# Optimization experiments

Hardware: AMD Instinct MI355X
Metric: run time of the kernel (lower is better)

## Reference

```python
import jax, jax.numpy as jnp
import numpy as np

B, S, D, H = 4, 2048, 1024, 16
HD = D // H


def setup_inputs() -> dict:
    key = jax.random.key(0)
    ks = jax.random.split(key, 10)
    x = jax.random.normal(ks[0], (B, S, D), dtype=jnp.float32)
    mask = jnp.zeros((B, 1, 1, S), dtype=jnp.float32)  # 1 = masked, 0 = keep
    sc = 1.0 / np.sqrt(D)
    wq = jax.random.normal(ks[1], (D, D), dtype=jnp.float32) * sc
    wk = jax.random.normal(ks[2], (D, D), dtype=jnp.float32) * sc
    wv = jax.random.normal(ks[3], (D, D), dtype=jnp.float32) * sc
    wo = jax.random.normal(ks[4], (D, D), dtype=jnp.float32) * sc
    bq = jnp.zeros((D,), jnp.float32)
    bk = jnp.zeros((D,), jnp.float32)
    bv = jnp.zeros((D,), jnp.float32)
    bo = jnp.zeros((D,), jnp.float32)
    return {"x": x, "mask": mask, "wq": wq, "bq": bq, "wk": wk, "bk": bk,
            "wv": wv, "bv": bv, "wo": wo, "bo": bo}


def _split_heads(t):
    # (B, S, D) -> (B, H, S, HD)
    return t.reshape(B, -1, H, HD).transpose(0, 2, 1, 3)


def reference(x, mask, wq, bq, wk, bk, wv, bv, wo, bo):
    q = _split_heads(x @ wq + bq)
    k = _split_heads(x @ wk + bk)
    v = _split_heads(x @ wv + bv)
    # scaled dot-product attention (TF tutorial convention: mask*-1e9 added)
    scores = jnp.einsum("bhqd,bhkd->bhqk", q, k) / jnp.sqrt(jnp.float32(HD))
    scores = scores + mask * -1e9
    attn_weights = jax.nn.softmax(scores, axis=-1)  # (B, H, Sq, Sk)
    attn = jnp.einsum("bhqk,bhkd->bhqd", attn_weights, v)
    attn = attn.transpose(0, 2, 1, 3).reshape(B, -1, D)
    out = attn @ wo + bo
    return out, attn_weights
```

## Files before the change

kernel.cpp:

```cpp
#include <hip/hip_runtime.h>
#include <hip/hip_bf16.h>

#define S_LEN  2048
#define DMODEL 1024
#define NHEAD  16
#define HDIM   64
#define BSZ    4

#define C_SCORE  0.18033688f
#define C_MASK  -1.4426950e9f

typedef __bf16 bf16_t;
typedef __bf16 bf16x8 __attribute__((ext_vector_type(8)));
typedef __bf16 bf16x4 __attribute__((ext_vector_type(4)));
typedef float  f32x4  __attribute__((ext_vector_type(4)));

typedef __attribute__((address_space(1))) void as1_void;
typedef __attribute__((address_space(3))) void as3_void;

__device__ __forceinline__ f32x4 mfma16(bf16x8 a, bf16x8 b, f32x4 c) {
    return __builtin_amdgcn_mfma_f32_16x16x32_bf16(a, b, c, 0, 0, 0);
}

__global__ __launch_bounds__(256) void cvt_all(const float* __restrict__ x,
                                               bf16_t* __restrict__ xb,
                                               const float* __restrict__ w0,
                                               const float* __restrict__ w1,
                                               const float* __restrict__ w2,
                                               const float* __restrict__ w3,
                                               bf16_t* __restrict__ wT) {
    __shared__ bf16_t t[64][65];
    const int bid = blockIdx.x;
    if (bid < 4096) {
        const int i0 = bid * 256 + threadIdx.x;
        #pragma unroll
        for (int rep = 0; rep < 2; ++rep) {
            const int i = i0 + rep * 1048576;
            float4 v = ((const float4*)x)[i];
            bf16x4 tv = { (bf16_t)v.x, (bf16_t)v.y, (bf16_t)v.z, (bf16_t)v.w };
            ((bf16x4*)xb)[i] = tv;
        }
        return;
    }
    const int wb = bid - 4096;
    const int wsel = wb >> 8;
    const float* w = wsel == 0 ? w0 : (wsel == 1 ? w1 : (wsel == 2 ? w2 : w3));
    bf16_t* wTo = wT + (size_t)wsel * DMODEL * DMODEL;
    const int rb = wb & 255;
    const int bx = (rb & 15) * 64, by = (rb >> 4) * 64;
    const int tx = threadIdx.x & 63, ty = threadIdx.x >> 6;
    #pragma unroll
    for (int rr = 0; rr < 64; rr += 4)
        t[tx][rr + ty] = (bf16_t)w[(size_t)(bx + rr + ty) * DMODEL + by + tx];
    __syncthreads();
    #pragma unroll
    for (int rr = 0; rr < 64; rr += 4)
        wTo[(size_t)(by + rr + ty) * DMODEL + bx + tx] = t[rr + ty][tx];
}

template <int MODE>
__global__ __launch_bounds__(256) void gemm_bt(const bf16_t* __restrict__ A,
                                               const bf16_t* __restrict__ Bt,
                                               const float* __restrict__ b0,
                                               const float* __restrict__ b1,
                                               const float* __restrict__ b2,
                                               bf16_t* __restrict__ o0,
                                               bf16_t* __restrict__ o1,
                                               bf16_t* __restrict__ o2,
                                               float* __restrict__ of) {
    constexpr int GK = 1024;
    __shared__ __attribute__((aligned(16))) bf16_t smem_ab[8704];
    bf16_t* As = smem_ab;
    bf16_t* Bs = smem_ab + 4096;

    const int tid  = threadIdx.x;
    const int wave = tid >> 6, lane = tid & 63;
    const int col16 = lane & 15, g = lane >> 4;
    const int wr = wave >> 1, wc = wave & 1;
    const int bn0 = blockIdx.x * 128, bm0 = blockIdx.y * 128;

    const int r4 = tid >> 2;
    const int c8 = (tid & 3) * 8;

    f32x4 acc[4][4] = {};

    for (int k0 = 0; k0 < GK; k0 += 32) {
        __syncthreads();
        #pragma unroll
        for (int i = 0; i < 2; ++i) {
            __builtin_amdgcn_global_load_lds(
                (const as1_void*)(A + (size_t)(bm0 + i * 64 + r4) * GK + k0 + c8),
                (as3_void*)(As + (i * 64 + wave * 16) * 32), 16, 0, 0);
            __builtin_amdgcn_global_load_lds(
                (const as1_void*)(Bt + (size_t)(bn0 + i * 64 + r4) * GK + k0 + c8),
                (as3_void*)(Bs + (i * 64 + wave * 16) * 32), 16, 0, 0);
        }
        __syncthreads();

        bf16x8 af[4], bfr[4];
        #pragma unroll
        for (int i = 0; i < 4; ++i) {
            af[i]  = *(const bf16x8*)(As + (wr * 64 + i * 16 + col16) * 32 + g * 8);
            bfr[i] = *(const bf16x8*)(Bs + (wc * 64 + i * 16 + col16) * 32 + g * 8);
        }
        #pragma unroll
        for (int mi = 0; mi < 4; ++mi)
            #pragma unroll
            for (int ni = 0; ni < 4; ++ni)
                acc[mi][ni] = mfma16(af[mi], bfr[ni], acc[mi][ni]);
    }

    if (MODE == 0 && (bn0 >> 10) == 2) {
        const int n1base = bn0 - 2048;
        const int brow = bm0 >> 11;
        const int s0 = bm0 & 2047;
        __syncthreads();
        #pragma unroll
        for (int p = 0; p < 2; ++p) {
            if (p) __syncthreads();
            if (wc == p) {
                #pragma unroll
                for (int ni = 0; ni < 4; ++ni) {
                    const float bv = b2[n1base + p * 64 + ni * 16 + col16];
                    #pragma unroll
                    for (int mi = 0; mi < 4; ++mi) {
                        bf16x4 pv;
                        #pragma unroll
                        for (int r = 0; r < 4; ++r) pv[r] = (bf16_t)(acc[mi][ni][r] + bv);
                        *(bf16x4*)&smem_ab[(ni * 16 + col16) * 136 + wr * 64 + mi * 16 + g * 4] = pv;
                    }
                }
            }
            __syncthreads();
            const int h2 = (n1base + p * 64) >> 6;
            bf16_t* vout = o2 + (((size_t)brow * NHEAD + h2) * HDIM) * S_LEN + s0;
            #pragma unroll
            for (int j = 0; j < 4; ++j) {
                const int unit = j * 256 + tid;
                const int row = unit >> 4;
                const int cu = (unit & 15) * 8;
                bf16x8 v = *(const bf16x8*)&smem_ab[row * 136 + cu];
                *(bf16x8*)(vout + (size_t)row * S_LEN + cu) = v;
            }
        }
        return;
    }

    #pragma unroll
    for (int ni = 0; ni < 4; ++ni) {
        const int gn = bn0 + wc * 64 + ni * 16 + col16;
        if (MODE == 0) {
            const int proj = bn0 >> 10;
            const float* bias = proj == 0 ? b0 : b1;
            bf16_t* outp      = proj == 0 ? o0 : o1;
            const int n1 = gn & 1023, h = n1 >> 6, hd = n1 & 63;
            const float bv = bias[n1];
            #pragma unroll
            for (int mi = 0; mi < 4; ++mi)
                #pragma unroll
                for (int r = 0; r < 4; ++r) {
                    const int gm = bm0 + wr * 64 + mi * 16 + g * 4 + r;
                    const int b = gm >> 11, s = gm & 2047;
                    outp[(((size_t)b * NHEAD + h) * S_LEN + s) * HDIM + hd] =
                        (bf16_t)(acc[mi][ni][r] + bv);
                }
        } else {
            const float bv = b0[gn];
            #pragma unroll
            for (int mi = 0; mi < 4; ++mi)
                #pragma unroll
                for (int r = 0; r < 4; ++r) {
                    const int gm = bm0 + wr * 64 + mi * 16 + g * 4 + r;
                    of[(size_t)gm * DMODEL + gn] = acc[mi][ni][r] + bv;
                }
        }
    }
}

__global__ __launch_bounds__(256, 2) void attn_fused(const bf16_t* __restrict__ Q,
                                                     const bf16_t* __restrict__ K,
                                                     const bf16_t* __restrict__ Vt,
                                                     const float* __restrict__ mask,
                                                     float* __restrict__ attnW,
                                                     bf16_t* __restrict__ ctx) {
    __shared__ __attribute__((aligned(16))) char smem[73728];
    bf16_t (*KsA)[128][64] = (bf16_t(*)[128][64])smem;
    bf16_t (*Ks)[64][64]   = (bf16_t(*)[64][64])smem;
    bf16_t (*Vs)[64][64]   = (bf16_t(*)[64][64])(smem + 16384);
    float  (*Pl)[32][64]   = (float(*)[32][64])(smem + 32768);
    float*  Ml             = (float*)(smem + 65536);

    const int tid = threadIdx.x, wave = tid >> 6, lane = tid & 63;
    const int col16 = lane & 15, g = lane >> 4;
    const int r7 = col16 & 7;

    const int lin = blockIdx.x;
    const int logical = (lin & 7) * 64 + (lin >> 3);
    const int bh = logical >> 3, pp = logical & 7;
    const int b = bh >> 4, h = bh & 15;
    const int qA = pp * 256 + wave * 32;
    const int qB = pp * 256 + 128 + wave * 32;

    const bf16_t* Qb = Q + (size_t)bh * S_LEN * HDIM;
    const bf16_t* Kb = K + (size_t)bh * S_LEN * HDIM;
    const bf16_t* Vb = Vt + (size_t)bh * HDIM * S_LEN;
    const float* mp = mask + (size_t)b * S_LEN;

    #pragma unroll
    for (int i = 0; i < 2; ++i) {
        const int idx = i * 256 + tid;
        f32x4 v = ((const f32x4*)mp)[idx];
        #pragma unroll
        for (int r = 0; r < 4; ++r) v[r] *= C_MASK;
        *(f32x4*)(&Ml[idx * 4]) = v;
    }

    const int srow  = lane >> 3;
    const int sunit = (lane & 7) ^ srow;

    auto stageA = [&](int buf, int it) {
        const int kk0 = it << 7;
        #pragma unroll
        for (int i2 = 0; i2 < 4; ++i2) {
            const int i = wave * 4 + i2;
            __builtin_amdgcn_global_load_lds(
                (const as1_void*)(Kb + (size_t)(kk0 + i * 8 + srow) * HDIM + sunit * 8),
                (as3_void*)(&KsA[buf][i * 8][0]), 16, 0, 0);
        }
    };
    auto stageK = [&](int buf, int it) {
        const int kk0 = it << 6;
        #pragma unroll
        for (int i2 = 0; i2 < 2; ++i2) {
            const int i = wave * 2 + i2;
            __builtin_amdgcn_global_load_lds(
                (const as1_void*)(Kb + (size_t)(kk0 + i * 8 + srow) * HDIM + sunit * 8),
                (as3_void*)(&Ks[buf][i * 8][0]), 16, 0, 0);
        }
    };
    auto stageV = [&](int buf, int it) {
        const int kk0 = it << 6;
        #pragma unroll
        for (int i2 = 0; i2 < 2; ++i2) {
            const int i = wave * 2 + i2;
            __builtin_amdgcn_global_load_lds(
                (const as1_void*)(Vb + (size_t)(i * 8 + srow) * S_LEN + kk0 + sunit * 8),
                (as3_void*)(&Vs[buf][i * 8][0]), 16, 0, 0);
        }
    };
    auto kfrag = [&](int buf, int nj, int kh) {
        return *(const bf16x8*)(&Ks[buf][nj * 16 + col16][(((kh * 4 + g) ^ r7) * 8)]);
    };
    auto vfrag = [&](int buf, int nd, int kh) {
        return *(const bf16x8*)(&Vs[buf][nd * 16 + col16][(((kh * 4 + g) ^ r7) * 8)]);
    };

    bf16x8 qa0[2][2], qa1[2][2];
    #pragma unroll
    for (int hh = 0; hh < 2; ++hh)
        #pragma unroll
        for (int kh = 0; kh < 2; ++kh) {
            qa0[hh][kh] = *(const bf16x8*)(Qb + (size_t)(qA + hh * 16 + col16) * HDIM +
                                           kh * 32 + g * 8);
            qa1[hh][kh] = *(const bf16x8*)(Qb + (size_t)(qB + hh * 16 + col16) * HDIM +
                                           kh * 32 + g * 8);
        }

    f32x4 lacc0[2] = {}, lacc1[2] = {};
    stageA(0, 0);
    __syncthreads();

    for (int it = 0; it < 16; ++it) {
        const int kk0 = it << 7, cur = it & 1;
        if (it < 15) stageA(cur ^ 1, it + 1);
        #pragma unroll
        for (int nj = 0; nj < 8; ++nj) {
            const f32x4 mvr = *(const f32x4*)(&Ml[kk0 + nj * 16 + g * 4]);
            const bf16x8 kf0 = *(const bf16x8*)(&KsA[cur][nj * 16 + col16][((g ^ r7) * 8)]);
            const bf16x8 kf1 = *(const bf16x8*)(&KsA[cur][nj * 16 + col16][(((4 + g) ^ r7) * 8)]);
            f32x4 t0 = {0.f, 0.f, 0.f, 0.f}, t1 = {0.f, 0.f, 0.f, 0.f};
            f32x4 u0 = {0.f, 0.f, 0.f, 0.f}, u1 = {0.f, 0.f, 0.f, 0.f};
            t0 = mfma16(kf0, qa0[0][0], t0);
            t0 = mfma16(kf1, qa0[0][1], t0);
            t1 = mfma16(kf0, qa0[1][0], t1);
            t1 = mfma16(kf1, qa0[1][1], t1);
            u0 = mfma16(kf0, qa1[0][0], u0);
            u0 = mfma16(kf1, qa1[0][1], u0);
            u1 = mfma16(kf0, qa1[1][0], u1);
            u1 = mfma16(kf1, qa1[1][1], u1);
            #pragma unroll
            for (int r = 0; r < 4; ++r) {
                lacc0[0][r] += exp2f(fmaf(t0[r], C_SCORE, mvr[r]));
                lacc0[1][r] += exp2f(fmaf(t1[r], C_SCORE, mvr[r]));
                lacc1[0][r] += exp2f(fmaf(u0[r], C_SCORE, mvr[r]));
                lacc1[1][r] += exp2f(fmaf(u1[r], C_SCORE, mvr[r]));
            }
        }
        asm volatile("s_waitcnt vmcnt(0)" ::: "memory");
        __builtin_amdgcn_sched_barrier(0);
        __builtin_amdgcn_s_barrier();
    }

    float crow0[2], crow1[2];
    #pragma unroll
    for (int hh = 0; hh < 2; ++hh) {
        float lr0 = (lacc0[hh][0] + lacc0[hh][1]) + (lacc0[hh][2] + lacc0[hh][3]);
        lr0 += __shfl_xor(lr0, 16);
        lr0 += __shfl_xor(lr0, 32);
        crow0[hh] = -__log2f(lr0);
        float lr1 = (lacc1[hh][0] + lacc1[hh][1]) + (lacc1[hh][2] + lacc1[hh][3]);
        lr1 += __shfl_xor(lr1, 16);
        lr1 += __shfl_xor(lr1, 32);
        crow1[hh] = -__log2f(lr1);
    }

    f32x4 o0[2][4] = {}, o1[2][4] = {};
    float* awA = attnW + ((size_t)bh * S_LEN + qA) * S_LEN;
    float* awB = attnW + ((size_t)bh * S_LEN + qB) * S_LEN;

    stageK(0, 0);
    stageV(0, 0);
    asm volatile("s_waitcnt vmcnt(0)" ::: "memory");
    __builtin_amdgcn_sched_barrier(0);
    __builtin_amdgcn_s_barrier();

    for (int it = 0; it < 32; ++it) {
        const int kk0 = it << 6, cur = it & 1;
        if (it < 31) { stageK(cur ^ 1, it + 1); stageV(cur ^ 1, it + 1); }
        __builtin_amdgcn_sched_barrier(0);
        f32x4 mvr[4];
        #pragma unroll
        for (int nj = 0; nj < 4; ++nj)
            mvr[nj] = *(const f32x4*)(&Ml[kk0 + nj * 16 + g * 4]);

        #pragma unroll
        for (int nj = 0; nj < 4; ++nj) {
            const bf16x8 kf0 = kfrag(cur, nj, 0);
            const bf16x8 kf1 = kfrag(cur, nj, 1);
            f32x4 s0 = {0.f, 0.f, 0.f, 0.f}, s1 = {0.f, 0.f, 0.f, 0.f};
            s0 = mfma16(kf0, qa0[0][0], s0);
            s0 = mfma16(kf1, qa0[0][1], s0);
            s1 = mfma16(kf0, qa0[1][0], s1);
            s1 = mfma16(kf1, qa0[1][1], s1);
            f32x4 pn0, pn1;
            #pragma unroll
            for (int r = 0; r < 4; ++r) {
                const float mm = mvr[nj][r];
                pn0[r] = exp2f(fmaf(s0[r], C_SCORE, mm + crow0[0]));
                pn1[r] = exp2f(fmaf(s1[r], C_SCORE, mm + crow0[1]));
            }
            const int pw = ((nj * 4 + g) ^ r7) * 4;
            *(f32x4*)(&Pl[wave][col16][pw])      = pn0;
            *(f32x4*)(&Pl[wave][16 + col16][pw]) = pn1;
        }
        #pragma unroll
        for (int j = 0; j < 8; ++j) {
            const int row = j * 4 + (lane >> 4);
            const int u = lane & 15;
            const f32x4 v = *(const f32x4*)(&Pl[wave][row][((u ^ (row & 7)) * 4)]);
            __builtin_nontemporal_store(v, (f32x4*)(awA + (size_t)row * S_LEN + kk0 + u * 4));
        }
        #pragma unroll
        for (int hh = 0; hh < 2; ++hh)
            #pragma unroll
            for (int kh = 0; kh < 2; ++kh) {
                const int u0i = kh * 8 + g * 2;
                const f32x4 a0 = *(const f32x4*)(&Pl[wave][hh * 16 + col16][((u0i ^ r7) * 4)]);
                const f32x4 a1 = *(const f32x4*)(&Pl[wave][hh * 16 + col16][(((u0i + 1) ^ r7) * 4)]);
                bf16x8 pa;
                #pragma unroll
                for (int j = 0; j < 4; ++j) {
                    pa[j]     = (bf16_t)a0[j];
                    pa[4 + j] = (bf16_t)a1[j];
                }
                #pragma unroll
                for (int nd = 0; nd < 4; ++nd)
                    o0[hh][nd] = mfma16(vfrag(cur, nd, kh), pa, o0[hh][nd]);
            }

        #pragma unroll
        for (int nj = 0; nj < 4; ++nj) {
            const bf16x8 kf0 = kfrag(cur, nj, 0);
            const bf16x8 kf1 = kfrag(cur, nj, 1);
            f32x4 s0 = {0.f, 0.f, 0.f, 0.f}, s1 = {0.f, 0.f, 0.f, 0.f};
            s0 = mfma16(kf0, qa1[0][0], s0);
            s0 = mfma16(kf1, qa1[0][1], s0);
            s1 = mfma16(kf0, qa1[1][0], s1);
            s1 = mfma16(kf1, qa1[1][1], s1);
            f32x4 pn0, pn1;
            #pragma unroll
            for (int r = 0; r < 4; ++r) {
                const float mm = mvr[nj][r];
                pn0[r] = exp2f(fmaf(s0[r], C_SCORE, mm + crow1[0]));
                pn1[r] = exp2f(fmaf(s1[r], C_SCORE, mm + crow1[1]));
            }
            const int pw = ((nj * 4 + g) ^ r7) * 4;
            *(f32x4*)(&Pl[wave][col16][pw])      = pn0;
            *(f32x4*)(&Pl[wave][16 + col16][pw]) = pn1;
        }
        #pragma unroll
        for (int j = 0; j < 8; ++j) {
            const int row = j * 4 + (lane >> 4);
            const int u = lane & 15;
            const f32x4 v = *(const f32x4*)(&Pl[wave][row][((u ^ (row & 7)) * 4)]);
            __builtin_nontemporal_store(v, (f32x4*)(awB + (size_t)row * S_LEN + kk0 + u * 4));
        }
        #pragma unroll
        for (int hh = 0; hh < 2; ++hh)
            #pragma unroll
            for (int kh = 0; kh < 2; ++kh) {
                const int u0i = kh * 8 + g * 2;
                const f32x4 a0 = *(const f32x4*)(&Pl[wave][hh * 16 + col16][((u0i ^ r7) * 4)]);
                const f32x4 a1 = *(const f32x4*)(&Pl[wave][hh * 16 + col16][(((u0i + 1) ^ r7) * 4)]);
                bf16x8 pa;
                #pragma unroll
                for (int j = 0; j < 4; ++j) {
                    pa[j]     = (bf16_t)a0[j];
                    pa[4 + j] = (bf16_t)a1[j];
                }
                #pragma unroll
                for (int nd = 0; nd < 4; ++nd)
                    o1[hh][nd] = mfma16(vfrag(cur, nd, kh), pa, o1[hh][nd]);
            }

        asm volatile("s_waitcnt vmcnt(16)" ::: "memory");
        __builtin_amdgcn_sched_barrier(0);
        __builtin_amdgcn_s_barrier();
    }

    #pragma unroll
    for (int hh = 0; hh < 2; ++hh) {
        bf16_t* cpA = ctx + ((size_t)b * S_LEN + qA + hh * 16 + col16) * DMODEL + h * HDIM;
        bf16_t* cpB = ctx + ((size_t)b * S_LEN + qB + hh * 16 + col16) * DMODEL + h * HDIM;
        #pragma unroll
        for (int nd = 0; nd < 4; ++nd) {
            bf16x4 cv0, cv1;
            #pragma unroll
            for (int r = 0; r < 4; ++r) {
                cv0[r] = (bf16_t)o0[hh][nd][r];
                cv1[r] = (bf16_t)o1[hh][nd][r];
            }
            *(bf16x4*)(cpA + nd * 16 + g * 4) = cv0;
            *(bf16x4*)(cpB + nd * 16 + g * 4) = cv1;
        }
    }
}

extern "C" void kernel_launch(void* const* d_in, const int* in_sizes, int n_in,
                              void* d_out, int out_size, void* d_ws, size_t ws_size,
                              hipStream_t stream) {
    const float* x    = (const float*)d_in[0];
    const float* mask = (const float*)d_in[1];
    const float* wq   = (const float*)d_in[2];
    const float* bq   = (const float*)d_in[3];
    const float* wk   = (const float*)d_in[4];
    const float* bk   = (const float*)d_in[5];
    const float* wv   = (const float*)d_in[6];
    const float* bv   = (const float*)d_in[7];
    const float* wo   = (const float*)d_in[8];
    const float* bo   = (const float*)d_in[9];

    const size_t nX = (size_t)BSZ * S_LEN * DMODEL;
    const size_t nW = (size_t)DMODEL * DMODEL;

    char* ws = (char*)d_ws;
    size_t off = 0;
    bf16_t* xb     = (bf16_t*)(ws + off); off += nX * 2;
    bf16_t* wqkvT  = (bf16_t*)(ws + off); off += 3 * nW * 2;
    bf16_t* woT    = (bf16_t*)(ws + off); off += nW * 2;
    bf16_t* qbh    = (bf16_t*)(ws + off); off += nX * 2;
    bf16_t* kbh    = (bf16_t*)(ws + off); off += nX * 2;
    bf16_t* vtb    = (bf16_t*)(ws + off); off += nX * 2;
    bf16_t* ctx    = (bf16_t*)(ws + off); off += nX * 2;
    if (ws_size < off) return;

    float* outp  = (float*)d_out;
    float* attnW = outp + nX;

    cvt_all<<<5120, 256, 0, stream>>>(x, xb, wq, wk, wv, wo, wqkvT);

    gemm_bt<0><<<dim3(24, 64), 256, 0, stream>>>(xb, wqkvT, bq, bk, bv,
                                                 qbh, kbh, vtb, nullptr);

    attn_fused<<<512, 256, 0, stream>>>(qbh, kbh, vtb, mask, attnW, ctx);

    gemm_bt<2><<<dim3(8, 64), 256, 0, stream>>>(ctx, woT, bo, nullptr, nullptr,
                                                nullptr, nullptr, nullptr, outp);
}
```

Measured before the change: 379.2 us.

## Split attention work across 8 waves with 16 query rows each

Doubles the attention block to 512 threads so each wave handles 16 query rows per half instead of 32. Global-to-LDS staging of K, V and the mask is spread across the eight waves, and the vmcnt wait is adjusted to match. The aim is lower per-wave register pressure and more waves to hide latency and overlap MFMA with exp work. The cost is that each K/V fragment read from LDS now feeds fewer MFMAs, raising LDS traffic. The tighter launch bounds also risk register spills.

New measurement: 369.0 us. 1.03x faster.

```diff
diff --git a/kernel.cpp b/kernel.cpp
--- a/kernel.cpp
+++ b/kernel.cpp
@@ -177,7 +177,7 @@
     }
 }
 
-__global__ __launch_bounds__(256, 2) void attn_fused(const bf16_t* __restrict__ Q,
+__global__ __launch_bounds__(512, 4) void attn_fused(const bf16_t* __restrict__ Q,
                                                      const bf16_t* __restrict__ K,
                                                      const bf16_t* __restrict__ Vt,
                                                      const float* __restrict__ mask,
@@ -187,7 +187,7 @@
     bf16_t (*KsA)[128][64] = (bf16_t(*)[128][64])smem;
     bf16_t (*Ks)[64][64]   = (bf16_t(*)[64][64])smem;
     bf16_t (*Vs)[64][64]   = (bf16_t(*)[64][64])(smem + 16384);
-    float  (*Pl)[32][64]   = (float(*)[32][64])(smem + 32768);
+    float  (*Pl)[16][64]   = (float(*)[16][64])(smem + 32768);
     float*  Ml             = (float*)(smem + 65536);
 
     const int tid = threadIdx.x, wave = tid >> 6, lane = tid & 63;
@@ -198,21 +198,19 @@
     const int logical = (lin & 7) * 64 + (lin >> 3);
     const int bh = logical >> 3, pp = logical & 7;
     const int b = bh >> 4, h = bh & 15;
-    const int qA = pp * 256 + wave * 32;
-    const int qB = pp * 256 + 128 + wave * 32;
+    const int qA = pp * 256 + wave * 16;
+    const int qB = pp * 256 + 128 + wave * 16;
 
     const bf16_t* Qb = Q + (size_t)bh * S_LEN * HDIM;
     const bf16_t* Kb = K + (size_t)bh * S_LEN * HDIM;
     const bf16_t* Vb = Vt + (size_t)bh * HDIM * S_LEN;
     const float* mp = mask + (size_t)b * S_LEN;
 
-    #pragma unroll
-    for (int i = 0; i < 2; ++i) {
-        const int idx = i * 256 + tid;
-        f32x4 v = ((const f32x4*)mp)[idx];
+    {
+        f32x4 v = ((const f32x4*)mp)[tid];
         #pragma unroll
         for (int r = 0; r < 4; ++r) v[r] *= C_MASK;
-        *(f32x4*)(&Ml[idx * 4]) = v;
+        *(f32x4*)(&Ml[tid * 4]) = v;
     }
 
     const int srow  = lane >> 3;
@@ -220,33 +218,25 @@
 
     auto stageA = [&](int buf, int it) {
         const int kk0 = it << 7;
-        #pragma unroll
-        for (int i2 = 0; i2 < 4; ++i2) {
-            const int i = wave * 4 + i2;
-            __builtin_amdgcn_global_load_lds(
-                (const as1_void*)(Kb + (size_t)(kk0 + i * 8 + srow) * HDIM + sunit * 8),
-                (as3_void*)(&KsA[buf][i * 8][0]), 16, 0, 0);
-        }
-    };
-    auto stageK = [&](int buf, int it) {
-        const int kk0 = it << 6;
         #pragma unroll
         for (int i2 = 0; i2 < 2; ++i2) {
             const int i = wave * 2 + i2;
             __builtin_amdgcn_global_load_lds(
                 (const as1_void*)(Kb + (size_t)(kk0 + i * 8 + srow) * HDIM + sunit * 8),
-                (as3_void*)(&Ks[buf][i * 8][0]), 16, 0, 0);
-        }
+                (as3_void*)(&KsA[buf][i * 8][0]), 16, 0, 0);
+        }
+    };
+    auto stageK = [&](int buf, int it) {
+        const int kk0 = it << 6;
+        __builtin_amdgcn_global_load_lds(
+            (const as1_void*)(Kb + (size_t)(kk0 + wave * 8 + srow) * HDIM + sunit * 8),
+            (as3_void*)(&Ks[buf][wave * 8][0]), 16, 0, 0);
     };
     auto stageV = [&](int buf, int it) {
         const int kk0 = it << 6;
-        #pragma unroll
-        for (int i2 = 0; i2 < 2; ++i2) {
-            const int i = wave * 2 + i2;
-            __builtin_amdgcn_global_load_lds(
-                (const as1_void*)(Vb + (size_t)(i * 8 + srow) * S_LEN + kk0 + sunit * 8),
-                (as3_void*)(&Vs[buf][i * 8][0]), 16, 0, 0);
-        }
+        __builtin_amdgcn_global_load_lds(
+            (const as1_void*)(Vb + (size_t)(wave * 8 + srow) * S_LEN + kk0 + sunit * 8),
+            (as3_void*)(&Vs[buf][wave * 8][0]), 16, 0, 0);
     };
     auto kfrag = [&](int buf, int nj, int kh) {
         return *(const bf16x8*)(&Ks[buf][nj * 16 + col16][(((kh * 4 + g) ^ r7) * 8)]);
@@ -255,18 +245,14 @@
         return *(const bf16x8*)(&Vs[buf][nd * 16 + col16][(((kh * 4 + g) ^ r7) * 8)]);
     };
 
-    bf16x8 qa0[2][2], qa1[2][2];
+    bf16x8 qa0[2], qa1[2];
     #pragma unroll
-    for (int hh = 0; hh < 2; ++hh)
-        #pragma unroll
-        for (int kh = 0; kh < 2; ++kh) {
-            qa0[hh][kh] = *(const bf16x8*)(Qb + (size_t)(qA + hh * 16 + col16) * HDIM +
-                                           kh * 32 + g * 8);
-            qa1[hh][kh] = *(const bf16x8*)(Qb + (size_t)(qB + hh * 16 + col16) * HDIM +
-                                           kh * 32 + g * 8);
-        }
-
-    f32x4 lacc0[2] = {}, lacc1[2] = {};
+    for (int kh = 0; kh < 2; ++kh) {
+        qa0[kh] = *(const bf16x8*)(Qb + (size_t)(qA + col16) * HDIM + kh * 32 + g * 8);
+        qa1[kh] = *(const bf16x8*)(Qb + (size_t)(qB + col16) * HDIM + kh * 32 + g * 8);
+    }
+
+    f32x4 lacc0 = {}, lacc1 = {};
     stageA(0, 0);
     __syncthreads();
 
@@ -278,22 +264,15 @@
             const f32x4 mvr = *(const f32x4*)(&Ml[kk0 + nj * 16 + g * 4]);
             const bf16x8 kf0 = *(const bf16x8*)(&KsA[cur][nj * 16 + col16][((g ^ r7) * 8)]);
             const bf16x8 kf1 = *(const bf16x8*)(&KsA[cur][nj * 16 + col16][(((4 + g) ^ r7) * 8)]);
-            f32x4 t0 = {0.f, 0.f, 0.f, 0.f}, t1 = {0.f, 0.f, 0.f, 0.f};
-            f32x4 u0 = {0.f, 0.f, 0.f, 0.f}, u1 = {0.f, 0.f, 0.f, 0.f};
-            t0 = mfma16(kf0, qa0[0][0], t0);
-            t0 = mfma16(kf1, qa0[0][1], t0);
-            t1 = mfma16(kf0, qa0[1][0], t1);
-            t1 = mfma16(kf1, qa0[1][1], t1);
-            u0 = mfma16(kf0, qa1[0][0], u0);
-            u0 = mfma16(kf1, qa1[0][1], u0);
-            u1 = mfma16(kf0, qa1[1][0], u1);
-            u1 = mfma16(kf1, qa1[1][1], u1);
+            f32x4 t0 = {0.f, 0.f, 0.f, 0.f}, u0 = {0.f, 0.f, 0.f, 0.f};
+            t0 = mfma16(kf0, qa0[0], t0);
+            t0 = mfma16(kf1, qa0[1], t0);
+            u0 = mfma16(kf0, qa1[0], u0);
+            u0 = mfma16(kf1, qa1[1], u0);
             #pragma unroll
             for (int r = 0; r < 4; ++r) {
-                lacc0[0][r] += exp2f(fmaf(t0[r], C_SCORE, mvr[r]));
-                lacc0[1][r] += exp2f(fmaf(t1[r], C_SCORE, mvr[r]));
-                lacc1[0][r] += exp2f(fmaf(u0[r], C_SCORE, mvr[r]));
-                lacc1[1][r] += exp2f(fmaf(u1[r], C_SCORE, mvr[r]));
+                lacc0[r] += exp2f(fmaf(t0[r], C_SCORE, mvr[r]));
+                lacc1[r] += exp2f(fmaf(u0[r], C_SCORE, mvr[r]));
             }
         }
         asm volatile("s_waitcnt vmcnt(0)" ::: "memory");
@@ -301,20 +280,19 @@
         __builtin_amdgcn_s_barrier();
     }
 
-    float crow0[2], crow1[2];
-    #pragma unroll
-    for (int hh = 0; hh < 2; ++hh) {
-        float lr0 = (lacc0[hh][0] + lacc0[hh][1]) + (lacc0[hh][2] + lacc0[hh][3]);
+    float crow0, crow1;
+    {
+        float lr0 = (lacc0[0] + lacc0[1]) + (lacc0[2] + lacc0[3]);
         lr0 += __shfl_xor(lr0, 16);
         lr0 += __shfl_xor(lr0, 32);
-        crow0[hh] = -__log2f(lr0);
-        float lr1 = (lacc1[hh][0] + lacc1[hh][1]) + (lacc1[hh][2] + lacc1[hh][3]);
+        crow0 = -__log2f(lr0);
+        float lr1 = (lacc1[0] + lacc1[1]) + (lacc1[2] + lacc1[3]);
         lr1 += __shfl_xor(lr1, 16);
         lr1 += __shfl_xor(lr1, 32);
-        crow1[hh] = -__log2f(lr1);
-    }
-
-    f32x4 o0[2][4] = {}, o1[2][4] = {};
+        crow1 = -__log2f(lr1);
+    }
+
+    f32x4 o0[4] = {}, o1[4] = {};
     float* awA = attnW + ((size_t)bh * S_LEN + qA) * S_LEN;
     float* awB = attnW + ((size_t)bh * S_LEN + qB) * S_LEN;
 
@@ -337,108 +315,89 @@
         for (int nj = 0; nj < 4; ++nj) {
             const bf16x8 kf0 = kfrag(cur, nj, 0);
             const bf16x8 kf1 = kfrag(cur, nj, 1);
-            f32x4 s0 = {0.f, 0.f, 0.f, 0.f}, s1 = {0.f, 0.f, 0.f, 0.f};
-            s0 = mfma16(kf0, qa0[0][0], s0);
-            s0 = mfma16(kf1, qa0[0][1], s0);
-            s1 = mfma16(kf0, qa0[1][0], s1);
-            s1 = mfma16(kf1, qa0[1][1], s1);
-            f32x4 pn0, pn1;
-            #pragma unroll
-            for (int r = 0; r < 4; ++r) {
-                const float mm = mvr[nj][r];
-                pn0[r] = exp2f(fmaf(s0[r], C_SCORE, mm + crow0[0]));
-                pn1[r] = exp2f(fmaf(s1[r], C_SCORE, mm + crow0[1]));
-            }
-            const int pw = ((nj * 4 + g) ^ r7) * 4;
-            *(f32x4*)(&Pl[wave][col16][pw])      = pn0;
-            *(f32x4*)(&Pl[wave][16 + col16][pw]) = pn1;
-        }
-        #pragma unroll
-        for (int j = 0; j < 8; ++j) {
+            f32x4 s0 = {0.f, 0.f, 0.f, 0.f};
+            s0 = mfma16(kf0, qa0[0], s0);
+            s0 = mfma16(kf1, qa0[1], s0);
+            f32x4 pn0;
+            #pragma unroll
+            for (int r = 0; r < 4; ++r)
+                pn0[r] = exp2f(fmaf(s0[r], C_SCORE, mvr[nj][r] + crow0));
+            *(f32x4*)(&Pl[wave][col16][(((nj * 4 + g) ^ r7) * 4)]) = pn0;
+        }
+        #pragma unroll
+        for (int j = 0; j < 4; ++j) {
             const int row = j * 4 + (lane >> 4);
             const int u = lane & 15;
             const f32x4 v = *(const f32x4*)(&Pl[wave][row][((u ^ (row & 7)) * 4)]);
             __builtin_nontemporal_store(v, (f32x4*)(awA + (size_t)row * S_LEN + kk0 + u * 4));
         }
         #pragma unroll
-        for (int hh = 0; hh < 2; ++hh)
-            #pragma unroll
-            for (int kh = 0; kh < 2; ++kh) {
-                const int u0i = kh * 8 + g * 2;
-                const f32x4 a0 = *(const f32x4*)(&Pl[wave][hh * 16 + col16][((u0i ^ r7) * 4)]);
-                const f32x4 a1 = *(const f32x4*)(&Pl[wave][hh * 16 + col16][(((u0i + 1) ^ r7) * 4)]);
-                bf16x8 pa;
-                #pragma unroll
-                for (int j = 0; j < 4; ++j) {
-                    pa[j]     = (bf16_t)a0[j];
-                    pa[4 + j] = (bf16_t)a1[j];
-                }
-                #pragma unroll
-                for (int nd = 0; nd < 4; ++nd)
-                    o0[hh][nd] = mfma16(vfrag(cur, nd, kh), pa, o0[hh][nd]);
-            }
+        for (int kh = 0; kh < 2; ++kh) {
+            const int u0i = kh * 8 + g * 2;
+            const f32x4 a0 = *(const f32x4*)(&Pl[wave][col16][((u0i ^ r7) * 4)]);
+            const f32x4 a1 = *(const f32x4*)(&Pl[wave][col16][(((u0i + 1) ^ r7) * 4)]);
+            bf16x8 pa;
+            #pragma unroll
+            for (int j = 0; j < 4; ++j) {
+                pa[j]     = (bf16_t)a0[j];
+                pa[4 + j] = (bf16_t)a1[j];
+            }
+            #pragma unroll
+            for (int nd = 0; nd < 4; ++nd)
+                o0[nd] = mfma16(vfrag(cur, nd, kh), pa, o0[nd]);
+        }
 
         #pragma unroll
         for (int nj = 0; nj < 4; ++nj) {
             const bf16x8 kf0 = kfrag(cur, nj, 0);
             const bf16x8 kf1 = kfrag(cur, nj, 1);
-            f32x4 s0 = {0.f, 0.f, 0.f, 0.f}, s1 = {0.f, 0.f, 0.f, 0.f};
-            s0 = mfma16(kf0, qa1[0][0], s0);
-            s0 = mfma16(kf1, qa1[0][1], s0);
-            s1 = mfma16(kf0, qa1[1][0], s1);
-            s1 = mfma16(kf1, qa1[1][1], s1);
-            f32x4 pn0, pn1;
-            #pragma unroll
-            for (int r = 0; r < 4; ++r) {
-                const float mm = mvr[nj][r];
-                pn0[r] = exp2f(fmaf(s0[r], C_SCORE, mm + crow1[0]));
-                pn1[r] = exp2f(fmaf(s1[r], C_SCORE, mm + crow1[1]));
-            }
-            const int pw = ((nj * 4 + g) ^ r7) * 4;
-            *(f32x4*)(&Pl[wave][col16][pw])      = pn0;
-            *(f32x4*)(&Pl[wave][16 + col16][pw]) = pn1;
-        }
-        #pragma unroll
-        for (int j = 0; j < 8; ++j) {
+            f32x4 s0 = {0.f, 0.f, 0.f, 0.f};
+            s0 = mfma16(kf0, qa1[0], s0);
+            s0 = mfma16(kf1, qa1[1], s0);
+            f32x4 pn0;
+            #pragma unroll
+            for (int r = 0; r < 4; ++r)
+                pn0[r] = exp2f(fmaf(s0[r], C_SCORE, mvr[nj][r] + crow1));
+            *(f32x4*)(&Pl[wave][col16][(((nj * 4 + g) ^ r7) * 4)]) = pn0;
+        }
+        #pragma unroll
+        for (int j = 0; j < 4; ++j) {
             const int row = j * 4 + (lane >> 4);
             const int u = lane & 15;
             const f32x4 v = *(const f32x4*)(&Pl[wave][row][((u ^ (row & 7)) * 4)]);
             __builtin_nontemporal_store(v, (f32x4*)(awB + (size_t)row * S_LEN + kk0 + u * 4));
         }
         #pragma unroll
-        for (int hh = 0; hh < 2; ++hh)
-            #pragma unroll
-            for (int kh = 0; kh < 2; ++kh) {
-                const int u0i = kh * 8 + g * 2;
-                const f32x4 a0 = *(const f32x4*)(&Pl[wave][hh * 16 + col16][((u0i ^ r7) * 4)]);
-                const f32x4 a1 = *(const f32x4*)(&Pl[wave][hh * 16 + col16][(((u0i + 1) ^ r7) * 4)]);
-                bf16x8 pa;
-                #pragma unroll
-                for (int j = 0; j < 4; ++j) {
-                    pa[j]     = (bf16_t)a0[j];
-                    pa[4 + j] = (bf16_t)a1[j];
-                }
-                #pragma unroll
-                for (int nd = 0; nd < 4; ++nd)
-                    o1[hh][nd] = mfma16(vfrag(cur, nd, kh), pa, o1[hh][nd]);
-            }
-
-        asm volatile("s_waitcnt vmcnt(16)" ::: "memory");
+        for (int kh = 0; kh < 2; ++kh) {
+            const int u0i = kh * 8 + g * 2;
+            const f32x4 a0 = *(const f32x4*)(&Pl[wave][col16][((u0i ^ r7) * 4)]);
+            const f32x4 a1 = *(const f32x4*)(&Pl[wave][col16][(((u0i + 1) ^ r7) * 4)]);
+            bf16x8 pa;
+            #pragma unroll
+            for (int j = 0; j < 4; ++j) {
+                pa[j]     = (bf16_t)a0[j];
+                pa[4 + j] = (bf16_t)a1[j];
+            }
+            #pragma unroll
+            for (int nd = 0; nd < 4; ++nd)
+                o1[nd] = mfma16(vfrag(cur, nd, kh), pa, o1[nd]);
+        }
+
+        asm volatile("s_waitcnt vmcnt(8)" ::: "memory");
         __builtin_amdgcn_sched_barrier(0);
         __builtin_amdgcn_s_barrier();
     }
 
-    #pragma unroll
-    for (int hh = 0; hh < 2; ++hh) {
-        bf16_t* cpA = ctx + ((size_t)b * S_LEN + qA + hh * 16 + col16) * DMODEL + h * HDIM;
-        bf16_t* cpB = ctx + ((size_t)b * S_LEN + qB + hh * 16 + col16) * DMODEL + h * HDIM;
+    {
+        bf16_t* cpA = ctx + ((size_t)b * S_LEN + qA + col16) * DMODEL + h * HDIM;
+        bf16_t* cpB = ctx + ((size_t)b * S_LEN + qB + col16) * DMODEL + h * HDIM;
         #pragma unroll
         for (int nd = 0; nd < 4; ++nd) {
             bf16x4 cv0, cv1;
             #pragma unroll
             for (int r = 0; r < 4; ++r) {
-                cv0[r] = (bf16_t)o0[hh][nd][r];
-                cv1[r] = (bf16_t)o1[hh][nd][r];
+                cv0[r] = (bf16_t)o0[nd][r];
+                cv1[r] = (bf16_t)o1[nd][r];
             }
             *(bf16x4*)(cpA + nd * 16 + g * 4) = cv0;
             *(bf16x4*)(cpB + nd * 16 + g * 4) = cv1;
@@ -482,7 +441,7 @@
     gemm_bt<0><<<dim3(24, 64), 256, 0, stream>>>(xb, wqkvT, bq, bk, bv,
                                                  qbh, kbh, vtb, nullptr);
 
-    attn_fused<<<512, 256, 0, stream>>>(qbh, kbh, vtb, mask, attnW, ctx);
+    attn_fused<<<512, 512, 0, stream>>>(qbh, kbh, vtb, mask, attnW, ctx);
 
     gemm_bt<2><<<dim3(8, 64), 256, 0, stream>>>(ctx, woT, bo, nullptr, nullptr,
                                                 nullptr, nullptr, nullptr, outp);
```
